# Performance work log

Measured on AMD Instinct MI355X. Metric: run time of the kernel, lower is better.

## Reference

```python
import jax, jax.numpy as jnp
import numpy as np
import math

B, L, H, D = 4, 2048, 8, 64
FACTOR = 5
SAMPLE_K = min(FACTOR * int(np.ceil(np.log(L))), L)  # U_part = 40
N_TOP = min(FACTOR * int(np.ceil(np.log(L))), L)     # u = 40


def setup_inputs() -> dict:
    key = jax.random.key(0)
    kq, kk, kv, ki = jax.random.split(key, 4)
    queries = jax.random.normal(kq, (B, L, H, D), dtype=jnp.float32)
    keys = jax.random.normal(kk, (B, L, H, D), dtype=jnp.float32)
    values = jax.random.normal(kv, (B, L, H, D), dtype=jnp.float32)
    # ProbSparse random key sampling indices (torch.randint(L_K, (L_Q, sample_k)))
    index_sample = jax.random.randint(ki, (L, SAMPLE_K), 0, L, dtype=jnp.int64)
    return {"queries": queries, "keys": keys, "values": values,
            "index_sample": index_sample}


def reference(queries, keys, values, index_sample):
    # [B, L, H, D] -> [B, H, L, D]
    Q = jnp.transpose(queries, (0, 2, 1, 3))
    K = jnp.transpose(keys, (0, 2, 1, 3))
    V = jnp.transpose(values, (0, 2, 1, 3))
    L_K = K.shape[2]

    # --- _prob_QK ---
    # gather sampled keys per query: [B, H, L_Q, sample_k, D]
    K_sample = K[:, :, index_sample, :]
    # sampled QK dots: [B, H, L_Q, sample_k]
    Q_K_sample = jnp.einsum('bhld,bhlsd->bhls', Q, K_sample)
    # sparsity measurement M = max - mean
    M = Q_K_sample.max(axis=-1) - Q_K_sample.sum(axis=-1) / L_K  # [B, H, L_Q]
    _, M_top = jax.lax.top_k(M, N_TOP)  # [B, H, n_top]
    # gather top queries: [B, H, n_top, D]
    Q_reduce = jnp.take_along_axis(Q, M_top[..., None], axis=2)
    # reduced scores against all keys: [B, H, n_top, L_K]
    scores_top = jnp.einsum('bhud,bhkd->bhuk', Q_reduce, K)

    # --- forward tail ---
    scale = 1.0 / math.sqrt(D)
    attn = jax.nn.softmax(scores_top * scale, axis=-1)  # dropout = identity (eval)
    context = jnp.einsum('bhuk,bhkd->bhud', attn, V)  # [B, H, n_top, D]
    # [B, n_top, H, D]
    return jnp.transpose(context, (0, 2, 1, 3))
```

## Files before the change

kernel.cpp:

```cpp
#include <hip/hip_runtime.h>
#include <hip/hip_bf16.h>

#define BB 4
#define LL 2048
#define HH 8
#define DD 64
#define SK 40
#define NT 40
#define CH 256
#define NCH (LL / CH)
#define QH 20

__global__ __launch_bounds__(256) void compute_m_kernel(
        const float* __restrict__ Q, const float* __restrict__ K,
        const int* __restrict__ idx, float* __restrict__ M) {
    __shared__ int sidx[SK];

    int blk = blockIdx.x;
    int x = blk & 7, g = blk >> 3;
    int b = x >> 1;
    int l = (g << 1) | (x & 1);
    int t = threadIdx.x;

    if (t < SK) sidx[t] = idx[(size_t)l * SK + t];

    int q  = t & 3;
    int h  = t >> 5;
    int s0 = (t >> 2) & 7;

    const float4* Qb = (const float4*)(Q + ((size_t)b * LL + l) * 512 + h * 64 + q * 16);
    float4 qf0 = Qb[0], qf1 = Qb[1], qf2 = Qb[2], qf3 = Qb[3];

    const float* Kb = K + (size_t)b * LL * 512 + h * 64 + q * 16;
    __syncthreads();

    const float4* src = (const float4*)(Kb + (size_t)sidx[s0] * 512);
    float4 k0 = src[0], k1 = src[1], k2 = src[2], k3 = src[3];

    float mx = -INFINITY, sm = 0.0f;
    #pragma unroll
    for (int p = 0; p < 5; ++p) {
        float4 c0 = k0, c1 = k1, c2 = k2, c3 = k3;
        if (p < 4) {
            const float4* s2 = (const float4*)(Kb + (size_t)sidx[(p + 1) * 8 + s0] * 512);
            k0 = s2[0]; k1 = s2[1]; k2 = s2[2]; k3 = s2[3];
        }
        float pd = qf0.x * c0.x + qf0.y * c0.y + qf0.z * c0.z + qf0.w * c0.w
                 + qf1.x * c1.x + qf1.y * c1.y + qf1.z * c1.z + qf1.w * c1.w
                 + qf2.x * c2.x + qf2.y * c2.y + qf2.z * c2.z + qf2.w * c2.w
                 + qf3.x * c3.x + qf3.y * c3.y + qf3.z * c3.z + qf3.w * c3.w;
        pd += __shfl_xor(pd, 1, 64);
        pd += __shfl_xor(pd, 2, 64);
        mx = fmaxf(mx, pd);
        sm += pd;
    }

    #pragma unroll
    for (int off = 16; off >= 1; off >>= 1) {
        mx = fmaxf(mx, __shfl_xor(mx, off, 64));
        sm += __shfl_xor(sm, off, 64);
    }
    if ((t & 31) == 0)
        M[((size_t)b * HH + h) * LL + l] = mx - sm * (1.0f / (4.0f * (float)LL));
}

__global__ __launch_bounds__(256) void topk_kernel(const float* __restrict__ M,
                                                   int* __restrict__ topi) {
    __shared__ unsigned long long keys[LL];
    __shared__ unsigned long long wmax[4];
    __shared__ int win;
    int bh = blockIdx.x;
    int t  = threadIdx.x;
    int lane = t & 63, w = t >> 6;

    unsigned long long kmax = 0ULL;
    #pragma unroll
    for (int j = 0; j < 8; ++j) {
        int i = t + 256 * j;
        unsigned int bits = __float_as_uint(M[(size_t)bh * LL + i]);
        bits = (bits & 0x80000000u) ? ~bits : (bits | 0x80000000u);
        unsigned long long k = ((unsigned long long)bits << 11)
                             | (unsigned int)(LL - 1 - i);
        keys[i] = k;
        if (k > kmax) kmax = k;
    }
    __syncthreads();

    for (int u = 0; u < NT; ++u) {
        unsigned long long k = kmax;
        #pragma unroll
        for (int off = 32; off >= 1; off >>= 1) {
            unsigned long long o = __shfl_xor(k, off, 64);
            if (o > k) k = o;
        }
        if (lane == 0) wmax[w] = k;
        __syncthreads();
        if (t == 0) {
            unsigned long long k0 = wmax[0], k1 = wmax[1], k2 = wmax[2], k3 = wmax[3];
            if (k1 > k0) k0 = k1;
            if (k3 > k2) k0 = (k3 > k0) ? k3 : k0; else if (k2 > k0) k0 = k2;
            if (k2 > k0) k0 = k2;
            if (k3 > k0) k0 = k3;
            int i = (LL - 1) - (int)(k0 & 0x7FF);
            topi[bh * NT + u] = i;
            keys[i] = 0ULL;
            win = i;
        }
        __syncthreads();
        if ((win & 255) == t) {
            kmax = 0ULL;
            #pragma unroll
            for (int j = 0; j < 8; ++j) {
                unsigned long long kk = keys[t + 256 * j];
                if (kk > kmax) kmax = kk;
            }
        }
    }
}

__global__ __launch_bounds__(256, 3) void attn_kernel(
        const float* __restrict__ Q, const float* __restrict__ K,
        const float* __restrict__ V, const int* __restrict__ topi,
        float2* __restrict__ pml, float* __restrict__ po) {
    __shared__ float  qs[QH][DD];
    __shared__ float4 e4buf[4][64];
    __shared__ float  oarea[4][QH][DD];
    __shared__ float  mlarea[4][QH][2];

    int blk = blockIdx.x;
    int qh  = blk >> 8;
    int cc2 = blk & 255;
    int c   = cc2 & (NCH - 1);
    int bh  = cc2 >> 3;
    int h = bh & (HH - 1), b = bh >> 3;
    int t = threadIdx.x, lane = t & 63, w = t >> 6;
    int u0 = qh * QH;

    for (int i = t; i < QH * DD; i += 256) {
        int u = i >> 6, d = i & 63;
        int lq = topi[bh * NT + u0 + u];
        qs[u][d] = Q[(((size_t)b * LL + lq) * HH + h) * DD + d];
    }

    int key = c * CH + w * 64 + lane;
    const float4* kr = (const float4*)&K[(((size_t)b * LL + key) * HH + h) * DD];
    float4 kreg[16];
    #pragma unroll
    for (int j = 0; j < 16; ++j) kreg[j] = kr[j];

    float vcol[64];
    const float* vb = &V[(((size_t)b * LL + c * CH + w * 64) * HH + h) * DD + lane];
    #pragma unroll
    for (int j = 0; j < 64; ++j) vcol[j] = vb[(size_t)j * HH * DD];

    __syncthreads();

    for (int uq = 0; uq < QH / 4; ++uq) {
        float o0 = 0, o1 = 0, o2 = 0, o3 = 0;
        float mv0, mv1, mv2, mv3, lv0, lv1, lv2, lv3;
        float4 ev;
        #pragma unroll
        for (int j = 0; j < 4; ++j) {
            int u = uq * 4 + j;
            const float4* q4 = (const float4*)&qs[u][0];
            float s = 0.0f;
            #pragma unroll
            for (int cc = 0; cc < 16; ++cc) {
                float4 qv = q4[cc];
                s += qv.x * kreg[cc].x + qv.y * kreg[cc].y
                   + qv.z * kreg[cc].z + qv.w * kreg[cc].w;
            }
            s *= 0.125f;
            float m = s;
            #pragma unroll
            for (int off = 32; off >= 1; off >>= 1)
                m = fmaxf(m, __shfl_xor(m, off, 64));
            float e = __expf(s - m);
            float ls = e;
            #pragma unroll
            for (int off = 32; off >= 1; off >>= 1)
                ls += __shfl_xor(ls, off, 64);
            if (j == 0) { mv0 = m; lv0 = ls; ev.x = e; }
            if (j == 1) { mv1 = m; lv1 = ls; ev.y = e; }
            if (j == 2) { mv2 = m; lv2 = ls; ev.z = e; }
            if (j == 3) { mv3 = m; lv3 = ls; ev.w = e; }
        }
        e4buf[w][lane] = ev;
        asm volatile("s_waitcnt lgkmcnt(0)" ::: "memory");
        #pragma unroll
        for (int l2 = 0; l2 < 64; ++l2) {
            float4 e = e4buf[w][l2];
            float  v = vcol[l2];
            o0 += e.x * v; o1 += e.y * v; o2 += e.z * v; o3 += e.w * v;
        }
        oarea[w][uq * 4 + 0][lane] = o0;
        oarea[w][uq * 4 + 1][lane] = o1;
        oarea[w][uq * 4 + 2][lane] = o2;
        oarea[w][uq * 4 + 3][lane] = o3;
        if (lane == 0) {
            mlarea[w][uq * 4 + 0][0] = mv0; mlarea[w][uq * 4 + 0][1] = lv0;
            mlarea[w][uq * 4 + 1][0] = mv1; mlarea[w][uq * 4 + 1][1] = lv1;
            mlarea[w][uq * 4 + 2][0] = mv2; mlarea[w][uq * 4 + 2][1] = lv2;
            mlarea[w][uq * 4 + 3][0] = mv3; mlarea[w][uq * 4 + 3][1] = lv3;
        }
    }
    __syncthreads();

    for (int i = t; i < QH * DD; i += 256) {
        int u = i >> 6, d = i & 63;
        float m0 = mlarea[0][u][0], m1 = mlarea[1][u][0];
        float m2 = mlarea[2][u][0], m3 = mlarea[3][u][0];
        float mb = fmaxf(fmaxf(m0, m1), fmaxf(m2, m3));
        float s0 = __expf(m0 - mb), s1 = __expf(m1 - mb);
        float s2 = __expf(m2 - mb), s3 = __expf(m3 - mb);
        float ob = oarea[0][u][d] * s0 + oarea[1][u][d] * s1
                 + oarea[2][u][d] * s2 + oarea[3][u][d] * s3;
        int gu = u0 + u;
        po[((size_t)(bh * NT + gu) * NCH + c) * DD + d] = ob;
        if (d == 0) {
            float lb = mlarea[0][u][1] * s0 + mlarea[1][u][1] * s1
                     + mlarea[2][u][1] * s2 + mlarea[3][u][1] * s3;
            pml[(bh * NT + gu) * NCH + c] = make_float2(mb, lb);
        }
    }
}

__global__ __launch_bounds__(256) void merge_kernel(
        const float2* __restrict__ pml, const float* __restrict__ po,
        float* __restrict__ out) {
    int wid  = blockIdx.x * 4 + (threadIdx.x >> 6);
    int lane = threadIdx.x & 63;
    int u  = wid % NT;
    int bh = wid / NT;
    int h = bh & (HH - 1), b = bh >> 3;
    int base = (bh * NT + u) * NCH;

    float m = -INFINITY;
    #pragma unroll
    for (int cc = 0; cc < NCH; ++cc) m = fmaxf(m, pml[base + cc].x);
    float lsum = 0.0f, o = 0.0f;
    #pragma unroll
    for (int cc = 0; cc < NCH; ++cc) {
        float2 ml = pml[base + cc];
        float sc = __expf(ml.x - m);
        lsum += ml.y * sc;
        o    += po[(size_t)(base + cc) * DD + lane] * sc;
    }
    out[(((size_t)b * NT + u) * HH + h) * DD + lane] = o / lsum;
}

extern "C" void kernel_launch(void* const* d_in, const int* in_sizes, int n_in,
                              void* d_out, int out_size, void* d_ws, size_t ws_size,
                              hipStream_t stream) {
    const float* Q   = (const float*)d_in[0];
    const float* K   = (const float*)d_in[1];
    const float* V   = (const float*)d_in[2];
    const int*   idx = (const int*)d_in[3];
    float* out = (float*)d_out;

    char* ws = (char*)d_ws;
    float*  M    = (float*)ws;                        ws += (size_t)BB * HH * LL * sizeof(float);
    int*    topi = (int*)ws;                          ws += (size_t)BB * HH * NT * sizeof(int);
    float2* pml  = (float2*)ws;                       ws += (size_t)BB * HH * NT * NCH * sizeof(float2);
    float*  po   = (float*)ws;

    hipLaunchKernelGGL(compute_m_kernel, dim3(BB * LL), dim3(256), 0, stream,
                       Q, K, idx, M);
    hipLaunchKernelGGL(topk_kernel, dim3(BB * HH), dim3(256), 0, stream, M, topi);
    hipLaunchKernelGGL(attn_kernel, dim3(2 * BB * HH * NCH), dim3(256), 0, stream,
                       Q, K, V, topi, pml, po);
    hipLaunchKernelGGL(merge_kernel, dim3(BB * HH * NT / 4), dim3(256), 0, stream,
                       pml, po, out);
}
```

Before: 197.9 us.

## Stage sampled K rows into LDS via async global_load_lds double buffering

The sampled-key gather in compute_m_kernel now copies full 512-float K rows (all heads) into a double-buffered LDS area using direct global-to-LDS loads. Threads then read their 16-float slice from LDS, with a barrier per phase. This replaces per-thread scattered register loads with whole-row coalesced transfers and overlaps the next phase's copy with the current dot products. It adds LDS usage and barriers. The top-k kernel's four-way max reduction is also simplified.

```diff
diff --git a/kernel.cpp b/kernel.cpp
--- a/kernel.cpp
+++ b/kernel.cpp
@@ -11,9 +11,18 @@
 #define NCH (LL / CH)
 #define QH 20
 
+#define NPH 5
+#define PH 8
+#define RS 516
+#define PBUF (PH * RS)
+
+typedef __attribute__((address_space(1))) const void* gl_ptr_t;
+typedef __attribute__((address_space(3))) void*       lds_ptr_t;
+
 __global__ __launch_bounds__(256) void compute_m_kernel(
         const float* __restrict__ Q, const float* __restrict__ K,
         const int* __restrict__ idx, float* __restrict__ M) {
+    __shared__ float kbuf[2 * PBUF];
     __shared__ int sidx[SK];
 
     int blk = blockIdx.x;
@@ -31,29 +40,48 @@
     const float4* Qb = (const float4*)(Q + ((size_t)b * LL + l) * 512 + h * 64 + q * 16);
     float4 qf0 = Qb[0], qf1 = Qb[1], qf2 = Qb[2], qf3 = Qb[3];
 
-    const float* Kb = K + (size_t)b * LL * 512 + h * 64 + q * 16;
-    __syncthreads();
-
-    const float4* src = (const float4*)(Kb + (size_t)sidx[s0] * 512);
-    float4 k0 = src[0], k1 = src[1], k2 = src[2], k3 = src[3];
+    const float* Kb = K + (size_t)b * LL * 512;
+
+    int wv   = t >> 6;
+    int lane = t & 63;
+    __syncthreads();
+
+    #define STAGE(p, buf) do {                                                  \
+        _Pragma("unroll")                                                       \
+        for (int i = 0; i < 4; ++i) {                                           \
+            int r  = wv * 2 + (i >> 1);                                         \
+            int hf = i & 1;                                                     \
+            const float* gsrc = Kb + (size_t)sidx[(p) * PH + r] * 512           \
+                              + hf * 256 + lane * 4;                            \
+            float* ldst = kbuf + (buf) * PBUF + r * RS + hf * 256;              \
+            __builtin_amdgcn_global_load_lds((gl_ptr_t)gsrc, (lds_ptr_t)ldst,   \
+                                             16, 0, 0);                         \
+        }                                                                       \
+    } while (0)
+
+    STAGE(0, 0);
+    __syncthreads();
 
     float mx = -INFINITY, sm = 0.0f;
     #pragma unroll
-    for (int p = 0; p < 5; ++p) {
-        float4 c0 = k0, c1 = k1, c2 = k2, c3 = k3;
-        if (p < 4) {
-            const float4* s2 = (const float4*)(Kb + (size_t)sidx[(p + 1) * 8 + s0] * 512);
-            k0 = s2[0]; k1 = s2[1]; k2 = s2[2]; k3 = s2[3];
-        }
-        float pd = qf0.x * c0.x + qf0.y * c0.y + qf0.z * c0.z + qf0.w * c0.w
-                 + qf1.x * c1.x + qf1.y * c1.y + qf1.z * c1.z + qf1.w * c1.w
-                 + qf2.x * c2.x + qf2.y * c2.y + qf2.z * c2.z + qf2.w * c2.w
-                 + qf3.x * c3.x + qf3.y * c3.y + qf3.z * c3.z + qf3.w * c3.w;
+    for (int p = 0; p < NPH; ++p) {
+        if (p < NPH - 1) STAGE(p + 1, (p + 1) & 1);
+        const float* kb = kbuf + (p & 1) * PBUF + s0 * RS + h * 64 + q * 16;
+        float4 k0 = *(const float4*)(kb);
+        float4 k1 = *(const float4*)(kb + 4);
+        float4 k2 = *(const float4*)(kb + 8);
+        float4 k3 = *(const float4*)(kb + 12);
+        float pd = qf0.x * k0.x + qf0.y * k0.y + qf0.z * k0.z + qf0.w * k0.w
+                 + qf1.x * k1.x + qf1.y * k1.y + qf1.z * k1.z + qf1.w * k1.w
+                 + qf2.x * k2.x + qf2.y * k2.y + qf2.z * k2.z + qf2.w * k2.w
+                 + qf3.x * k3.x + qf3.y * k3.y + qf3.z * k3.z + qf3.w * k3.w;
         pd += __shfl_xor(pd, 1, 64);
         pd += __shfl_xor(pd, 2, 64);
         mx = fmaxf(mx, pd);
         sm += pd;
-    }
+        if (p < NPH - 1) __syncthreads();
+    }
+    #undef STAGE
 
     #pragma unroll
     for (int off = 16; off >= 1; off >>= 1) {
@@ -96,11 +124,10 @@
         if (lane == 0) wmax[w] = k;
         __syncthreads();
         if (t == 0) {
-            unsigned long long k0 = wmax[0], k1 = wmax[1], k2 = wmax[2], k3 = wmax[3];
-            if (k1 > k0) k0 = k1;
-            if (k3 > k2) k0 = (k3 > k0) ? k3 : k0; else if (k2 > k0) k0 = k2;
-            if (k2 > k0) k0 = k2;
-            if (k3 > k0) k0 = k3;
+            unsigned long long k0 = wmax[0];
+            if (wmax[1] > k0) k0 = wmax[1];
+            if (wmax[2] > k0) k0 = wmax[2];
+            if (wmax[3] > k0) k0 = wmax[3];
             int i = (LL - 1) - (int)(k0 & 0x7FF);
             topi[bh * NT + u] = i;
             keys[i] = 0ULL;
```

Measured after the change: 177.4 us. 1.12x faster.
